# Performance work log

Hardware: AMD Instinct MI355X
Metric: run time of the kernel (lower is better)

The kernel has to match this reference:

```python
import jax, jax.numpy as jnp
import numpy as np

D_MODEL = 768
D_INNER = 1536
D_STATE = 16
D_CONV = 4
DT_RANK = 48
N_LAYER = 4
VOCAB = 32000
B, L = 2, 1024


def rmsnorm(x, w, eps=1e-5):
    return x * jax.lax.rsqrt(jnp.mean(x * x, axis=-1, keepdims=True) + eps) * w


def depthwise_causal_conv(u, w):
    # u: (b, l, d_in), w: (d_in, k). torch pads both sides then truncates to l,
    # which equals left-pad by k-1 (causal).
    b, l, d = u.shape
    k = w.shape[1]
    up = jnp.pad(u, ((0, 0), (k - 1, 0), (0, 0)))
    out = jnp.zeros_like(u)
    for i in range(k):
        out = out + up[:, i:i + l, :] * w[:, i]
    return out


def selective_scan(u, delta, A, Bm, C, Dp):
    # u,delta: (b,l,d_in); A: (d_in,n); Bm,C: (b,l,n); Dp: (d_in,)
    dA = jnp.exp(delta[..., None] * A)                      # (b,l,d,n)
    dBu = delta[..., None] * Bm[:, :, None, :] * u[..., None]

    def step(h, inp):
        dA_t, dBu_t, C_t = inp
        h = dA_t * h + dBu_t                                 # (b,d,n)
        y = jnp.einsum('bdn,bn->bd', h, C_t)
        return h, y

    h0 = jnp.zeros_like(dA[:, 0])
    xs = (jnp.moveaxis(dA, 1, 0), jnp.moveaxis(dBu, 1, 0), jnp.moveaxis(C, 1, 0))
    _, ys = jax.lax.scan(step, h0, xs)                       # (l,b,d)
    return jnp.moveaxis(ys, 0, 1) + u * Dp


def setup_inputs() -> dict:
    key = jax.random.key(0)
    ks = jax.random.split(key, 16)
    s = lambda fan: 1.0 / np.sqrt(fan)
    inp = {}
    inp['text_input'] = jax.random.randint(ks[0], (B, L), 0, VOCAB)
    inp['visual_input'] = jax.random.normal(ks[1], (B, L, D_MODEL), dtype=jnp.float32)
    inp['embedding'] = jax.random.normal(ks[2], (VOCAB, D_MODEL), dtype=jnp.float32) * 0.02
    inp['norm_w'] = jnp.ones((N_LAYER, D_MODEL), dtype=jnp.float32)
    inp['norm_f_w'] = jnp.ones((D_MODEL,), dtype=jnp.float32)
    inp['in_proj_w'] = jax.random.normal(ks[3], (N_LAYER, 2 * D_INNER, D_MODEL)) * s(D_MODEL)
    inp['in_proj2_w'] = jax.random.normal(ks[4], (N_LAYER, D_INNER, D_MODEL)) * s(D_MODEL)
    inp['conv_w'] = jax.random.normal(ks[5], (N_LAYER, D_INNER, D_CONV)) * s(D_CONV)
    inp['conv_b'] = jax.random.normal(ks[6], (N_LAYER, D_INNER)) * 0.01
    inp['x_proj_w'] = jax.random.normal(ks[7], (N_LAYER, DT_RANK + D_STATE, D_INNER)) * s(D_INNER)
    inp['c_proj_w'] = jax.random.normal(ks[8], (N_LAYER, D_STATE, D_INNER)) * s(D_INNER)
    inp['dt_proj_w'] = jax.random.normal(ks[9], (N_LAYER, D_INNER, DT_RANK)) * s(DT_RANK)
    inp['dt_proj_b'] = jax.random.normal(ks[10], (N_LAYER, D_INNER)) * 0.01
    A = jnp.tile(jnp.arange(1, D_STATE + 1, dtype=jnp.float32)[None, :], (D_INNER, 1))
    inp['A_log'] = jnp.tile(jnp.log(A)[None], (N_LAYER, 1, 1))
    inp['D'] = jnp.ones((N_LAYER, D_INNER), dtype=jnp.float32)
    inp['out_proj_w'] = jax.random.normal(ks[11], (N_LAYER, D_MODEL, D_INNER)) * s(D_INNER)
    return inp


def reference(text_input, visual_input, embedding, norm_w, norm_f_w, in_proj_w,
              in_proj2_w, conv_w, conv_b, x_proj_w, c_proj_w, dt_proj_w,
              dt_proj_b, A_log, D, out_proj_w):
    x = embedding[text_input]  # (b,l,d_model)
    n_layer = A_log.shape[0]
    l = x.shape[1]
    for i in range(n_layer):
        q = rmsnorm(x, norm_w[i])
        v = rmsnorm(visual_input, norm_w[i])
        xr = q @ in_proj_w[i].T                               # (b,l,2*d_inner)
        vin = v @ in_proj2_w[i].T                             # (b,l,d_inner)
        t, res = jnp.split(xr, 2, axis=-1)
        t = depthwise_causal_conv(t, conv_w[i]) + conv_b[i]
        t = jax.nn.silu(t)
        # ssm
        A = -jnp.exp(A_log[i])
        x_dbl = t @ x_proj_w[i].T                             # (b,l,dt_rank+n)
        delta, Bm = jnp.split(x_dbl, [DT_RANK], axis=-1)
        C = vin @ c_proj_w[i].T                               # (b,l,n)
        delta = jax.nn.softplus(delta @ dt_proj_w[i].T + dt_proj_b[i])
        y = selective_scan(t, delta, A, Bm, C, D[i])
        y = y * jax.nn.silu(res)
        x = y @ out_proj_w[i].T + x
    x = rmsnorm(x, norm_f_w)
    return x @ embedding.T  # tied lm_head -> (b,l,vocab)
```

## Files before the change

### kernel.cpp

```cpp
#include <hip/hip_runtime.h>
#include <hip/hip_bf16.h>
#include <math.h>

#define B_ 2
#define L_ 1024
#define DM 768
#define DI 1536
#define DS 16
#define DR 48
#define NL 4
#define VOC 32000
#define BL (B_*L_)
#define NCH 32
#define LCH (L_/NCH)
#define NXD 80
#define DTILE 8

typedef __attribute__((ext_vector_type(8))) short short8;
typedef __attribute__((ext_vector_type(4))) float f32x4;

__device__ __forceinline__ float sigmoidf_(float x){ return 1.f/(1.f+expf(-x)); }
__device__ __forceinline__ float siluf_(float x){ return x*sigmoidf_(x); }
__device__ __forceinline__ float softplusf_(float x){ return fmaxf(x,0.f) + log1pf(expf(-fabsf(x))); }
__device__ __forceinline__ unsigned short f2bf(float f){
    unsigned u = __float_as_uint(f);
    u += 0x7FFFu + ((u >> 16) & 1u);
    return (unsigned short)(u >> 16);
}
__device__ __forceinline__ float bf2f(unsigned short h){
    return __uint_as_float((unsigned)h << 16);
}
__device__ __forceinline__ void gload_lds16(const unsigned short* g, unsigned short* l){
    __builtin_amdgcn_global_load_lds(
        (const __attribute__((address_space(1))) void*)g,
        (__attribute__((address_space(3))) void*)l, 16, 0, 0);
}
__device__ __forceinline__ short8 lds_frag(const unsigned short* buf, int row, int kb){
    return *(const short8*)&buf[row*64 + ((kb ^ (row & 7)) << 3)];
}

__global__ void cast_bf16_kernel(const float* __restrict__ in, unsigned short* __restrict__ out, int n4)
{
    for (int i = blockIdx.x*256 + threadIdx.x; i < n4; i += gridDim.x*256) {
        float4 v = ((const float4*)in)[i];
        ushort4 o;
        o.x = f2bf(v.x); o.y = f2bf(v.y); o.z = f2bf(v.z); o.w = f2bf(v.w);
        ((ushort4*)out)[i] = o;
    }
}

__global__ void embed_kernel(const int* __restrict__ idx, const float* __restrict__ emb,
                             float* __restrict__ x)
{
    int i = blockIdx.x*256 + threadIdx.x;
    if (i >= BL*DM) return;
    int c = i % DM; int bl = i / DM;
    x[i] = emb[(size_t)idx[bl]*DM + c];
}

__global__ void rmsnorm_bf_kernel(const float* __restrict__ in, const float* __restrict__ w,
                                  unsigned short* __restrict__ out)
{
    int row = blockIdx.x;
    const float* xr = in + (size_t)row*DM;
    float ss = 0.f;
    for (int c = threadIdx.x; c < DM; c += 256) { float v = xr[c]; ss += v*v; }
    #pragma unroll
    for (int o = 32; o > 0; o >>= 1) ss += __shfl_down(ss, o, 64);
    __shared__ float red[4];
    if ((threadIdx.x & 63) == 0) red[threadIdx.x >> 6] = ss;
    __syncthreads();
    float tot = red[0] + red[1] + red[2] + red[3];
    float scale = rsqrtf(tot * (1.f/DM) + 1e-5f);
    for (int c = threadIdx.x; c < DM; c += 256)
        out[(size_t)row*DM + c] = f2bf(xr[c]*scale*w[c]);
}

__global__ void prep_layer(
    const float* __restrict__ x, const float* __restrict__ vis, const float* __restrict__ w,
    unsigned short* __restrict__ qh, unsigned short* __restrict__ ql,
    unsigned short* __restrict__ vh, unsigned short* __restrict__ vl,
    const float* __restrict__ s1, unsigned short* __restrict__ h1, unsigned short* __restrict__ l1, int n1,
    const float* __restrict__ s2, unsigned short* __restrict__ h2, unsigned short* __restrict__ l2, int n2,
    const float* __restrict__ s3, unsigned short* __restrict__ h3, unsigned short* __restrict__ l3, int n3)
{
    if (blockIdx.x < 2*BL) {
        int row = blockIdx.x;
        bool first = row < BL;
        int r = first ? row : row - BL;
        const float* xr = (first ? x : vis) + (size_t)r*DM;
        unsigned short* oh = (first ? qh : vh) + (size_t)r*DM;
        unsigned short* ol = (first ? ql : vl) + (size_t)r*DM;
        float ss = 0.f;
        for (int c = threadIdx.x; c < DM; c += 256) { float v = xr[c]; ss += v*v; }
        #pragma unroll
        for (int o = 32; o > 0; o >>= 1) ss += __shfl_down(ss, o, 64);
        __shared__ float red[4];
        if ((threadIdx.x & 63) == 0) red[threadIdx.x >> 6] = ss;
        __syncthreads();
        float tot = red[0] + red[1] + red[2] + red[3];
        float scale = rsqrtf(tot * (1.f/DM) + 1e-5f);
        for (int c = threadIdx.x; c < DM; c += 256) {
            float v = xr[c]*scale*w[c];
            unsigned short h = f2bf(v);
            oh[c] = h;
            ol[c] = f2bf(v - bf2f(h));
        }
    } else {
        int total = n1 + n2 + n3;
        int nblk = gridDim.x - 2*BL;
        for (int i = (blockIdx.x - 2*BL)*256 + threadIdx.x; i < total; i += nblk*256) {
            const float* s; unsigned short *h, *l; int j;
            if (i < n1)           { s = s1; h = h1; l = l1; j = i; }
            else if (i < n1 + n2) { s = s2; h = h2; l = l2; j = i - n1; }
            else                  { s = s3; h = h3; l = l3; j = i - n1 - n2; }
            float4 v = ((const float4*)s)[j];
            ushort4 hh, ll;
            hh.x = f2bf(v.x); ll.x = f2bf(v.x - bf2f(hh.x));
            hh.y = f2bf(v.y); ll.y = f2bf(v.y - bf2f(hh.y));
            hh.z = f2bf(v.z); ll.z = f2bf(v.z - bf2f(hh.z));
            hh.w = f2bf(v.w); ll.w = f2bf(v.w - bf2f(hh.w));
            ((ushort4*)h)[j] = hh;
            ((ushort4*)l)[j] = ll;
        }
    }
}

__global__ __launch_bounds__(512) void gemm_head8(
    const unsigned short* __restrict__ A, int lda,
    const unsigned short* __restrict__ W, int ldb,
    float* __restrict__ C, int ldc, int K)
{
    __shared__ unsigned short As[2][256*64];
    __shared__ unsigned short Bs[2][256*64];
    const int tid = threadIdx.x;
    const int bm = blockIdx.y*256, bn = blockIdx.x*256;
    const int l  = tid & 63;
    const int w  = tid >> 6;
    const int wm = w >> 2, wn = w & 3;
    const int lr = l & 15, lg = l >> 4;

    auto stage = [&](int t, int db) {
        int k0 = t*64;
        #pragma unroll
        for (int i = 0; i < 4; i++) {
            int c = i*512 + tid;
            int row = c >> 3, kb = c & 7;
            int kbs = (kb ^ (row & 7)) << 3;
            gload_lds16(A + (size_t)(bm+row)*lda + k0 + kbs, &As[db][c*8]);
        }
        #pragma unroll
        for (int i = 0; i < 4; i++) {
            int c = i*512 + tid;
            int row = c >> 3, kb = c & 7;
            int kbs = (kb ^ (row & 7)) << 3;
            gload_lds16(W + (size_t)(bn+row)*ldb + k0 + kbs, &Bs[db][c*8]);
        }
    };

    f32x4 zero4 = {0.f, 0.f, 0.f, 0.f};
    f32x4 acc[8][4];
    #pragma unroll
    for (int m = 0; m < 8; m++)
        #pragma unroll
        for (int n = 0; n < 4; n++) acc[m][n] = zero4;

    const int NT = K/64;
    stage(0, 0);
    stage(1, 1);

    for (int t = 0; t < NT; t++) {
        int cur = t & 1;
        if (t + 1 < NT) { asm volatile("s_waitcnt vmcnt(8)" ::: "memory"); }
        else            { asm volatile("s_waitcnt vmcnt(0)" ::: "memory"); }
        __builtin_amdgcn_s_barrier();
        __builtin_amdgcn_sched_barrier(0);

        const unsigned short* Ab = As[cur];
        const unsigned short* Bb = Bs[cur];
        short8 bf0[4], bf1[4];
        #pragma unroll
        for (int n = 0; n < 4; n++) {
            int row = wn*64 + n*16 + lr;
            bf0[n] = lds_frag(Bb, row, lg);
            bf1[n] = lds_frag(Bb, row, 4 + lg);
        }
        #pragma unroll
        for (int m = 0; m < 8; m++) {
            int row = wm*128 + m*16 + lr;
            short8 a0 = lds_frag(Ab, row, lg);
            short8 a1 = lds_frag(Ab, row, 4 + lg);
            __builtin_amdgcn_s_setprio(1);
            #pragma unroll
            for (int n = 0; n < 4; n++) {
                acc[m][n] = __builtin_amdgcn_mfma_f32_16x16x32_bf16(a0, bf0[n], acc[m][n], 0, 0, 0);
                acc[m][n] = __builtin_amdgcn_mfma_f32_16x16x32_bf16(a1, bf1[n], acc[m][n], 0, 0, 0);
            }
            __builtin_amdgcn_s_setprio(0);
        }
        __builtin_amdgcn_sched_barrier(0);
        __builtin_amdgcn_s_barrier();
        if (t + 2 < NT) stage(t + 2, cur);
    }

    #pragma unroll
    for (int m = 0; m < 8; m++)
        #pragma unroll
        for (int n = 0; n < 4; n++) {
            int col = bn + wn*64 + n*16 + lr;
            #pragma unroll
            for (int r = 0; r < 4; r++) {
                int rowi = bm + wm*128 + m*16 + lg*4 + r;
                C[(size_t)rowi*ldc + col] = acc[m][n][r];
            }
        }
}

__global__ __launch_bounds__(512) void gemm_mfma2p_dual(
    const unsigned short* __restrict__ Ah1, const unsigned short* __restrict__ Al1,
    const unsigned short* __restrict__ Wh1, const unsigned short* __restrict__ Wl1,
    float* __restrict__ C1, int ldc1, int nb1,
    const unsigned short* __restrict__ Ah2, const unsigned short* __restrict__ Al2,
    const unsigned short* __restrict__ Wh2, const unsigned short* __restrict__ Wl2,
    float* __restrict__ C2, int ldc2,
    int lda, int ldb, int K)
{
    __shared__ unsigned short AsH[2][128*64];
    __shared__ unsigned short AsL[2][128*64];
    __shared__ unsigned short BsH[2][128*64];
    __shared__ unsigned short BsL[2][128*64];
    const int tid = threadIdx.x;
    const int bx = blockIdx.x;
    const bool first = bx < nb1;
    const unsigned short* Ah = first ? Ah1 : Ah2;
    const unsigned short* Al = first ? Al1 : Al2;
    const unsigned short* Wh = first ? Wh1 : Wh2;
    const unsigned short* Wl = first ? Wl1 : Wl2;
    float* C  = first ? C1 : C2;
    const int ldc = first ? ldc1 : ldc2;
    const int bn = (first ? bx : bx - nb1)*128;
    const int bm = blockIdx.y*128;
    const int l  = tid & 63;
    const int w  = tid >> 6;
    const int wm = w >> 2, wn = w & 3;
    const int lr = l & 15, lg = l >> 4;

    auto stage = [&](int t, int db) {
        int k0 = t*64;
        #pragma unroll
        for (int i = 0; i < 2; i++) {
            int c = i*512 + tid;
            int row = c >> 3, kb = c & 7;
            int kbs = (kb ^ (row & 7)) << 3;
            const size_t ao = (size_t)(bm+row)*lda + k0 + kbs;
            const size_t bo = (size_t)(bn+row)*ldb + k0 + kbs;
            gload_lds16(Ah + ao, &AsH[db][c*8]);
            gload_lds16(Al + ao, &AsL[db][c*8]);
            gload_lds16(Wh + bo, &BsH[db][c*8]);
            gload_lds16(Wl + bo, &BsL[db][c*8]);
        }
    };

    f32x4 zero4 = {0.f, 0.f, 0.f, 0.f};
    f32x4 acc[4][2];
    #pragma unroll
    for (int m = 0; m < 4; m++)
        #pragma unroll
        for (int n = 0; n < 2; n++) acc[m][n] = zero4;

    const int NT = K/64;
    stage(0, 0);
    stage(1, 1);

    for (int t = 0; t < NT; t++) {
        int cur = t & 1;
        if (t + 1 < NT) { asm volatile("s_waitcnt vmcnt(8)" ::: "memory"); }
        else            { asm volatile("s_waitcnt vmcnt(0)" ::: "memory"); }
        __builtin_amdgcn_s_barrier();
        __builtin_amdgcn_sched_barrier(0);

        const unsigned short* AbH = AsH[cur];
        const unsigned short* AbL = AsL[cur];
        const unsigned short* BbH = BsH[cur];
        const unsigned short* BbL = BsL[cur];

        #pragma unroll
        for (int kk = 0; kk < 2; kk++) {
            short8 ah[4], al[4], bh[2], bl[2];
            #pragma unroll
            for (int m = 0; m < 4; m++) {
                int row = wm*64 + m*16 + lr;
                ah[m] = lds_frag(AbH, row, kk*4 + lg);
                al[m] = lds_frag(AbL, row, kk*4 + lg);
            }
            #pragma unroll
            for (int n = 0; n < 2; n++) {
                int row = wn*32 + n*16 + lr;
                bh[n] = lds_frag(BbH, row, kk*4 + lg);
                bl[n] = lds_frag(BbL, row, kk*4 + lg);
            }
            __builtin_amdgcn_s_setprio(1);
            #pragma unroll
            for (int m = 0; m < 4; m++)
                #pragma unroll
                for (int n = 0; n < 2; n++) {
                    acc[m][n] = __builtin_amdgcn_mfma_f32_16x16x32_bf16(al[m], bh[n], acc[m][n], 0, 0, 0);
                    acc[m][n] = __builtin_amdgcn_mfma_f32_16x16x32_bf16(ah[m], bl[n], acc[m][n], 0, 0, 0);
                    acc[m][n] = __builtin_amdgcn_mfma_f32_16x16x32_bf16(ah[m], bh[n], acc[m][n], 0, 0, 0);
                }
            __builtin_amdgcn_s_setprio(0);
        }
        __builtin_amdgcn_sched_barrier(0);
        __builtin_amdgcn_s_barrier();
        if (t + 2 < NT) stage(t + 2, cur);
    }

    #pragma unroll
    for (int m = 0; m < 4; m++)
        #pragma unroll
        for (int n = 0; n < 2; n++) {
            int col = bn + wn*32 + n*16 + lr;
            #pragma unroll
            for (int r = 0; r < 4; r++) {
                int rowi = bm + wm*64 + m*16 + lg*4 + r;
                C[(size_t)rowi*ldc + col] = acc[m][n][r];
            }
        }
}

template<int EPI>
__device__ __forceinline__ void mfma2_body(
    const unsigned short* __restrict__ Ah, const unsigned short* __restrict__ Alo, int lda,
    const unsigned short* __restrict__ Wh, const unsigned short* __restrict__ Wlo, int ldb,
    float* __restrict__ C, int ldc, const float* __restrict__ extra,
    int K, int bm, int bn,
    unsigned short* Ash, unsigned short* Asl, unsigned short* Bsh, unsigned short* Bsl)
{
    const int tid = threadIdx.x;
    const int l  = tid & 63;
    const int w  = tid >> 6;
    const int wr = (w >> 1)*64, wc = (w & 1)*64;
    const int lr = l & 15, lg = l >> 4;

    f32x4 zero4 = {0.f, 0.f, 0.f, 0.f};
    f32x4 acc[4][4];
    #pragma unroll
    for (int m = 0; m < 4; m++)
        #pragma unroll
        for (int n = 0; n < 4; n++) acc[m][n] = zero4;

    for (int k0 = 0; k0 < K; k0 += 64) {
        __syncthreads();
        #pragma unroll
        for (int i = 0; i < 4; i++) {
            int c   = i*256 + tid;
            int row = c >> 3;
            int kb  = c & 7;
            int kbs = (kb ^ (row & 7)) << 3;
            const size_t ao = (size_t)(bm+row)*lda + k0 + kbs;
            const size_t bo = (size_t)(bn+row)*ldb + k0 + kbs;
            gload_lds16(Ah  + ao, &Ash[c*8]);
            gload_lds16(Alo + ao, &Asl[c*8]);
            gload_lds16(Wh  + bo, &Bsh[c*8]);
            gload_lds16(Wlo + bo, &Bsl[c*8]);
        }
        __syncthreads();
        #pragma unroll
        for (int kk = 0; kk < 2; kk++) {
            short8 ah[4], al[4], bh[4], bl[4];
            #pragma unroll
            for (int m = 0; m < 4; m++) {
                int row = wr + m*16 + lr;
                ah[m] = lds_frag(Ash, row, kk*4 + lg);
                al[m] = lds_frag(Asl, row, kk*4 + lg);
            }
            #pragma unroll
            for (int n = 0; n < 4; n++) {
                int row = wc + n*16 + lr;
                bh[n] = lds_frag(Bsh, row, kk*4 + lg);
                bl[n] = lds_frag(Bsl, row, kk*4 + lg);
            }
            #pragma unroll
            for (int m = 0; m < 4; m++)
                #pragma unroll
                for (int n = 0; n < 4; n++) {
                    acc[m][n] = __builtin_amdgcn_mfma_f32_16x16x32_bf16(al[m], bh[n], acc[m][n], 0, 0, 0);
                    acc[m][n] = __builtin_amdgcn_mfma_f32_16x16x32_bf16(ah[m], bl[n], acc[m][n], 0, 0, 0);
                    acc[m][n] = __builtin_amdgcn_mfma_f32_16x16x32_bf16(ah[m], bh[n], acc[m][n], 0, 0, 0);
                }
        }
    }

    #pragma unroll
    for (int m = 0; m < 4; m++)
        #pragma unroll
        for (int n = 0; n < 4; n++) {
            int col = bn + wc + n*16 + lr;
            #pragma unroll
            for (int r = 0; r < 4; r++) {
                int rowi = bm + wr + m*16 + lg*4 + r;
                float v = acc[m][n][r];
                if (EPI == 1) v += extra[(size_t)rowi*ldc + col];
                C[(size_t)rowi*ldc + col] = v;
            }
        }
}

template<int EPI>
__global__ __launch_bounds__(256) void gemm_mfma2(
    const unsigned short* __restrict__ Ah, const unsigned short* __restrict__ Alo, int lda,
    const unsigned short* __restrict__ Wh, const unsigned short* __restrict__ Wlo, int ldb,
    float* __restrict__ C, int ldc, const float* __restrict__ extra, int K)
{
    __shared__ unsigned short Ash[128*64];
    __shared__ unsigned short Asl[128*64];
    __shared__ unsigned short Bsh[128*64];
    __shared__ unsigned short Bsl[128*64];
    mfma2_body<EPI>(Ah, Alo, lda, Wh, Wlo, ldb, C, ldc, extra, K,
                    blockIdx.y*128, blockIdx.x*128, Ash, Asl, Bsh, Bsl);
}

template<int EPI>
__global__ __launch_bounds__(256) void gemm_tile(
    const float* __restrict__ A, int lda,
    const float* __restrict__ W, int ldb,
    float* __restrict__ C, int ldc,
    const float* __restrict__ extra,
    int K)
{
    __shared__ float As[8][128];
    __shared__ float Bs[8][128];
    const int bm = blockIdx.y * 128;
    const int bn = blockIdx.x * 128;
    const int tid = threadIdx.x;
    const int lr = tid >> 1;
    const int lh = (tid & 1) * 4;
    const int tr = tid >> 4;
    const int tc = tid & 15;

    float acc[8][8];
    #pragma unroll
    for (int i = 0; i < 8; i++)
        #pragma unroll
        for (int j = 0; j < 8; j++) acc[i][j] = 0.f;

    const float* Arow = A + (size_t)(bm + lr)*lda + lh;
    const float* Wrow = W + (size_t)(bn + lr)*ldb + lh;

    for (int k0 = 0; k0 < K; k0 += 8) {
        float4 av = *(const float4*)(Arow + k0);
        float4 wv = *(const float4*)(Wrow + k0);
        __syncthreads();
        As[lh+0][lr] = av.x; As[lh+1][lr] = av.y; As[lh+2][lr] = av.z; As[lh+3][lr] = av.w;
        Bs[lh+0][lr] = wv.x; Bs[lh+1][lr] = wv.y; Bs[lh+2][lr] = wv.z; Bs[lh+3][lr] = wv.w;
        __syncthreads();
        #pragma unroll
        for (int k = 0; k < 8; k++) {
            float a[8], b[8];
            *(float4*)(a)   = *(const float4*)&As[k][tr*8];
            *(float4*)(a+4) = *(const float4*)&As[k][tr*8+4];
            *(float4*)(b)   = *(const float4*)&Bs[k][tc*8];
            *(float4*)(b+4) = *(const float4*)&Bs[k][tc*8+4];
            #pragma unroll
            for (int i = 0; i < 8; i++)
                #pragma unroll
                for (int j = 0; j < 8; j++)
                    acc[i][j] = fmaf(a[i], b[j], acc[i][j]);
        }
    }

    #pragma unroll
    for (int i = 0; i < 8; i++) {
        int row = bm + tr*8 + i;
        float* crow = C + (size_t)row*ldc + bn + tc*8;
        float v[8];
        if (EPI == 2) {
            const float* bia = extra + bn + tc*8;
            #pragma unroll
            for (int j = 0; j < 8; j++) v[j] = softplusf_(acc[i][j] + bia[j]);
        } else {
            #pragma unroll
            for (int j = 0; j < 8; j++) v[j] = acc[i][j];
        }
        *(float4*)(crow)   = make_float4(v[0],v[1],v[2],v[3]);
        *(float4*)(crow+4) = make_float4(v[4],v[5],v[6],v[7]);
    }
}

__global__ __launch_bounds__(256) void gemm_skinny2(
    const float* __restrict__ A1, const float* __restrict__ A2, int lda,
    const float* __restrict__ W1, const float* __restrict__ W2, int ldb,
    float* __restrict__ outx, int K)
{
    __shared__ float As[64][36];
    __shared__ float Ws[16][36];
    int tid = threadIdx.x;
    int bx = blockIdx.x;
    bool isC = (bx == 4);
    const float* A = isC ? A2 : A1;
    const float* W = isC ? W2 : W1;
    int bn = isC ? 0 : bx*16;
    int colbase = isC ? 64 : bx*16;
    int bm = blockIdx.y*64;
    int ar = tid >> 2, ak = (tid & 3)*8;
    int wr = tid >> 4, wk = (tid & 15)*2;
    int tr = tid >> 4, tc = tid & 15;

    float acc[4] = {0.f,0.f,0.f,0.f};
    for (int k0 = 0; k0 < K; k0 += 32) {
        float4 a0 = *(const float4*)(A + (size_t)(bm+ar)*lda + k0 + ak);
        float4 a1 = *(const float4*)(A + (size_t)(bm+ar)*lda + k0 + ak + 4);
        float2 wv = *(const float2*)(W + (size_t)(bn+wr)*ldb + k0 + wk);
        __syncthreads();
        *(float4*)&As[ar][ak]   = a0;
        *(float4*)&As[ar][ak+4] = a1;
        Ws[wr][wk] = wv.x; Ws[wr][wk+1] = wv.y;
        __syncthreads();
        #pragma unroll
        for (int k = 0; k < 32; k += 4) {
            float4 wv4 = *(const float4*)&Ws[tc][k];
            #pragma unroll
            for (int i = 0; i < 4; i++) {
                float4 av4 = *(const float4*)&As[tr*4+i][k];
                acc[i] = fmaf(av4.x, wv4.x, acc[i]);
                acc[i] = fmaf(av4.y, wv4.y, acc[i]);
                acc[i] = fmaf(av4.z, wv4.z, acc[i]);
                acc[i] = fmaf(av4.w, wv4.w, acc[i]);
            }
        }
    }
    #pragma unroll
    for (int i = 0; i < 4; i++)
        outx[(size_t)(bm + tr*4 + i)*NXD + colbase + tc] = acc[i];
}

__global__ void conv_silu_kernel(const float* __restrict__ xr, const float* __restrict__ cw,
                                 const float* __restrict__ cb, float* __restrict__ t)
{
    int i = blockIdx.x*256 + threadIdx.x;
    if (i >= BL*DI) return;
    int d = i % DI; int bl = i / DI; int l = bl % L_; int b = bl / L_;
    const float* base = xr + (size_t)b*L_*(2*DI);
    float acc = cb[d];
    #pragma unroll
    for (int q = 0; q < 4; q++) {
        int ll = l - 3 + q;
        if (ll >= 0) acc = fmaf(base[(size_t)ll*(2*DI) + d], cw[d*4+q], acc);
    }
    t[i] = siluf_(acc);
}

__global__ __launch_bounds__(256) void scan_fused(
    const float* __restrict__ delta, const float* __restrict__ t,
    const float* __restrict__ xdbl,
    const float* __restrict__ A_log, const float* __restrict__ Dp,
    const float* __restrict__ xr,
    unsigned short* __restrict__ zh, unsigned short* __restrict__ zl)
{
    __shared__ float P_lds[256*17];
    __shared__ float S_lds[256*17];
    int blk = blockIdx.x;
    int b  = blk / (DI/DTILE);
    int d0 = (blk % (DI/DTILE))*DTILE;
    int tid = threadIdx.x;
    int dl = tid & (DTILE-1), c = tid / DTILE;
    int d = d0 + dl;

    float Ad[16];
    #pragma unroll
    for (int n = 0; n < 16; n++) Ad[n] = -expf(A_log[d*16+n]);

    float P[16], S[16];
    #pragma unroll
    for (int n = 0; n < 16; n++) { P[n] = 1.f; S[n] = 0.f; }
    for (int s = 0; s < LCH; s++) {
        int bl = b*L_ + c*LCH + s;
        float dt = delta[(size_t)bl*DI + d];
        float u  = t[(size_t)bl*DI + d];
        const float4* Bp4 = (const float4*)(xdbl + (size_t)bl*NXD + 48);
        float Bv[16];
        #pragma unroll
        for (int q = 0; q < 4; q++) {
            float4 bv = Bp4[q];
            Bv[q*4+0]=bv.x; Bv[q*4+1]=bv.y; Bv[q*4+2]=bv.z; Bv[q*4+3]=bv.w;
        }
        float du = dt*u;
        #pragma unroll
        for (int n = 0; n < 16; n++) {
            float a = expf(dt*Ad[n]);
            P[n] *= a;
            S[n] = fmaf(a, S[n], du*Bv[n]);
        }
    }
    #pragma unroll
    for (int n = 0; n < 16; n++) { P_lds[tid*17+n] = P[n]; S_lds[tid*17+n] = S[n]; }
    __syncthreads();

    if (tid < DTILE*16) {
        int dl2 = tid >> 4, n2 = tid & 15;
        float h = 0.f;
        for (int cc = 0; cc < NCH; cc++) {
            int slot = cc*DTILE + dl2;
            float p = P_lds[slot*17 + n2];
            float s = S_lds[slot*17 + n2];
            S_lds[slot*17 + n2] = h;
            h = fmaf(p, h, s);
        }
    }
    __syncthreads();

    float h[16];
    #pragma unroll
    for (int n = 0; n < 16; n++) h[n] = S_lds[tid*17+n];
    float Dd = Dp[d];
    for (int s = 0; s < LCH; s++) {
        int bl = b*L_ + c*LCH + s;
        float dt = delta[(size_t)bl*DI + d];
        float u  = t[(size_t)bl*DI + d];
        const float4* Bp4 = (const float4*)(xdbl + (size_t)bl*NXD + 48);
        const float4* Cp4 = (const float4*)(xdbl + (size_t)bl*NXD + 64);
        float Bv[16], Cv[16];
        #pragma unroll
        for (int q = 0; q < 4; q++) {
            float4 bv = Bp4[q]; float4 cv = Cp4[q];
            Bv[q*4+0]=bv.x; Bv[q*4+1]=bv.y; Bv[q*4+2]=bv.z; Bv[q*4+3]=bv.w;
            Cv[q*4+0]=cv.x; Cv[q*4+1]=cv.y; Cv[q*4+2]=cv.z; Cv[q*4+3]=cv.w;
        }
        float du = dt*u;
        float y = 0.f;
        #pragma unroll
        for (int n = 0; n < 16; n++) {
            float a = expf(dt*Ad[n]);
            h[n] = fmaf(a, h[n], du*Bv[n]);
            y = fmaf(h[n], Cv[n], y);
        }
        y = fmaf(u, Dd, y);
        float r = xr[(size_t)bl*(2*DI) + DI + d];
        float zv = y * siluf_(r);
        unsigned short hh = f2bf(zv);
        zh[(size_t)bl*DI + d] = hh;
        zl[(size_t)bl*DI + d] = f2bf(zv - bf2f(hh));
    }
}

extern "C" void kernel_launch(void* const* d_in, const int* in_sizes, int n_in,
                              void* d_out, int out_size, void* d_ws, size_t ws_size,
                              hipStream_t stream)
{
    const int*   text     = (const int*)  d_in[0];
    const float* visual   = (const float*)d_in[1];
    const float* emb      = (const float*)d_in[2];
    const float* norm_w   = (const float*)d_in[3];
    const float* norm_f_w = (const float*)d_in[4];
    const float* in_proj  = (const float*)d_in[5];
    const float* in_proj2 = (const float*)d_in[6];
    const float* conv_w   = (const float*)d_in[7];
    const float* conv_b   = (const float*)d_in[8];
    const float* x_proj   = (const float*)d_in[9];
    const float* c_proj   = (const float*)d_in[10];
    const float* dt_w     = (const float*)d_in[11];
    const float* dt_b     = (const float*)d_in[12];
    const float* A_log    = (const float*)d_in[13];
    const float* Dp       = (const float*)d_in[14];
    const float* out_proj = (const float*)d_in[15];
    float* out = (float*)d_out;

    float* ws = (float*)d_ws;
    size_t off = 0;
    float* x     = ws + off; off += (size_t)BL*DM;
    float* xr    = ws + off; off += (size_t)BL*2*DI;
    float* vin   = ws + off; off += (size_t)BL*DI;
    float* tb    = ws + off; off += (size_t)BL*DI;
    float* dl    = ws + off; off += (size_t)BL*DI;
    float* xdbl  = ws + off; off += (size_t)BL*NXD;

    unsigned short* bfb = (unsigned short*)(ws + off);
    size_t bo = 0;
    unsigned short* emb_bf = bfb + bo; bo += (size_t)VOC*DM;
    unsigned short* wA_h   = bfb + bo; bo += (size_t)2*DI*DM;
    unsigned short* wA_l   = bfb + bo; bo += (size_t)2*DI*DM;
    unsigned short* wB_h   = bfb + bo; bo += (size_t)DI*DM;
    unsigned short* wB_l   = bfb + bo; bo += (size_t)DI*DM;
    unsigned short* wO_h   = bfb + bo; bo += (size_t)DM*DI;
    unsigned short* wO_l   = bfb + bo; bo += (size_t)DM*DI;
    unsigned short* q_h    = bfb + bo; bo += (size_t)BL*DM;
    unsigned short* q_l    = bfb + bo; bo += (size_t)BL*DM;
    unsigned short* v_h    = bfb + bo; bo += (size_t)BL*DM;
    unsigned short* v_l    = bfb + bo; bo += (size_t)BL*DM;
    unsigned short* z_h    = bfb + bo; bo += (size_t)BL*DI;
    unsigned short* z_l    = bfb + bo; bo += (size_t)BL*DI;
    unsigned short* xn_bf  = bfb + bo; bo += (size_t)BL*DM;

    dim3 blk(256);

    cast_bf16_kernel<<<dim3(2048), blk, 0, stream>>>(emb, emb_bf, VOC*DM/4);

    embed_kernel<<<dim3((BL*DM)/256), blk, 0, stream>>>(text, emb, x);

    for (int i = 0; i < NL; i++) {
        const float* nw = norm_w + (size_t)i*DM;

        prep_layer<<<dim3(2*BL + 1024), blk, 0, stream>>>(
            x, visual, nw, q_h, q_l, v_h, v_l,
            in_proj  + (size_t)i*2*DI*DM, wA_h, wA_l, 2*DI*DM/4,
            in_proj2 + (size_t)i*DI*DM,   wB_h, wB_l, DI*DM/4,
            out_proj + (size_t)i*DM*DI,   wO_h, wO_l, DM*DI/4);

        gemm_mfma2p_dual<<<dim3(2*DI/128 + DI/128, BL/128), dim3(512), 0, stream>>>(
            q_h, q_l, wA_h, wA_l, xr, 2*DI, 2*DI/128,
            v_h, v_l, wB_h, wB_l, vin, DI,
            DM, DM, DM);

        conv_silu_kernel<<<dim3((BL*DI)/256), blk, 0, stream>>>(
            xr, conv_w + (size_t)i*DI*4, conv_b + (size_t)i*DI, tb);

        gemm_skinny2<<<dim3(5, BL/64), blk, 0, stream>>>(
            tb, vin, DI, x_proj + (size_t)i*(DR+DS)*DI, c_proj + (size_t)i*DS*DI, DI,
            xdbl, DI);

        gemm_tile<2><<<dim3(DI/128, BL/128), blk, 0, stream>>>(
            xdbl, NXD, dt_w + (size_t)i*DI*DR, DR, dl, DI, dt_b + (size_t)i*DI, DR);

        scan_fused<<<dim3(B_*DI/DTILE), blk, 0, stream>>>(
            dl, tb, xdbl, A_log + (size_t)i*DI*DS, Dp + (size_t)i*DI, xr, z_h, z_l);

        gemm_mfma2<1><<<dim3(DM/128, BL/128), blk, 0, stream>>>(
            z_h, z_l, DI, wO_h, wO_l, DI, x, DM, x, DI);
    }

    rmsnorm_bf_kernel<<<dim3(BL), blk, 0, stream>>>(x, norm_f_w, xn_bf);
    gemm_head8<<<dim3(VOC/256, BL/256), dim3(512), 0, stream>>>(
        xn_bf, DM, emb_bf, DM, out, VOC, DM);
}
```

Measured before the change: 1.589 ms.

## Fuse causal conv+SiLU into skinny GEMM and scan, drop separate conv kernel

Removes the standalone depthwise causal conv + SiLU kernel and its intermediate buffer. The x_proj skinny GEMM now loads xr tiles with a 3-row halo into LDS and computes conv+SiLU on the fly. The scan kernel recomputes the conv output from xr in both passes. This saves one launch and a write plus reread of the BL*DI intermediate. In exchange the scan does four strided xr reads and a sigmoid per step, twice, and the GEMM gets an extra sync and more work per tile.

```diff
diff --git a/kernel.cpp b/kernel.cpp
--- a/kernel.cpp
+++ b/kernel.cpp
@@ -488,16 +488,20 @@
 }
 
 __global__ __launch_bounds__(256) void gemm_skinny2(
-    const float* __restrict__ A1, const float* __restrict__ A2, int lda,
+    const float* __restrict__ xr,
+    const float* __restrict__ vin,
+    const float* __restrict__ cw, const float* __restrict__ cb,
     const float* __restrict__ W1, const float* __restrict__ W2, int ldb,
     float* __restrict__ outx, int K)
 {
-    __shared__ float As[64][36];
+    __shared__ float Ar[68][36];
+    __shared__ float Ac[64][36];
     __shared__ float Ws[16][36];
+    __shared__ float cwS[32][4];
+    __shared__ float cbS[32];
     int tid = threadIdx.x;
     int bx = blockIdx.x;
     bool isC = (bx == 4);
-    const float* A = isC ? A2 : A1;
     const float* W = isC ? W2 : W1;
     int bn = isC ? 0 : bx*16;
     int colbase = isC ? 64 : bx*16;
@@ -505,23 +509,66 @@
     int ar = tid >> 2, ak = (tid & 3)*8;
     int wr = tid >> 4, wk = (tid & 15)*2;
     int tr = tid >> 4, tc = tid & 15;
+    bool halo_ok = (bm % L_) != 0;
 
     float acc[4] = {0.f,0.f,0.f,0.f};
     for (int k0 = 0; k0 < K; k0 += 32) {
-        float4 a0 = *(const float4*)(A + (size_t)(bm+ar)*lda + k0 + ak);
-        float4 a1 = *(const float4*)(A + (size_t)(bm+ar)*lda + k0 + ak + 4);
+        float4 a0, a1, h0, h1, cwv;
+        float cbv = 0.f;
+        if (isC) {
+            a0 = *(const float4*)(vin + (size_t)(bm+ar)*DI + k0 + ak);
+            a1 = *(const float4*)(vin + (size_t)(bm+ar)*DI + k0 + ak + 4);
+        } else {
+            a0 = *(const float4*)(xr + (size_t)(bm+ar)*(2*DI) + k0 + ak);
+            a1 = *(const float4*)(xr + (size_t)(bm+ar)*(2*DI) + k0 + ak + 4);
+            if (tid < 12) {
+                if (halo_ok) {
+                    h0 = *(const float4*)(xr + (size_t)(bm-3+(tid>>2))*(2*DI) + k0 + (tid&3)*8);
+                    h1 = *(const float4*)(xr + (size_t)(bm-3+(tid>>2))*(2*DI) + k0 + (tid&3)*8 + 4);
+                } else {
+                    h0 = make_float4(0.f,0.f,0.f,0.f);
+                    h1 = make_float4(0.f,0.f,0.f,0.f);
+                }
+            }
+            if (tid < 32) {
+                cwv = *(const float4*)(cw + (size_t)(k0+tid)*4);
+                cbv = cb[k0+tid];
+            }
+        }
         float2 wv = *(const float2*)(W + (size_t)(bn+wr)*ldb + k0 + wk);
         __syncthreads();
-        *(float4*)&As[ar][ak]   = a0;
-        *(float4*)&As[ar][ak+4] = a1;
+        if (isC) {
+            *(float4*)&Ar[ar][ak]   = a0;
+            *(float4*)&Ar[ar][ak+4] = a1;
+        } else {
+            *(float4*)&Ar[3+ar][ak]   = a0;
+            *(float4*)&Ar[3+ar][ak+4] = a1;
+            if (tid < 12) {
+                *(float4*)&Ar[tid>>2][(tid&3)*8]     = h0;
+                *(float4*)&Ar[tid>>2][(tid&3)*8 + 4] = h1;
+            }
+            if (tid < 32) { *(float4*)&cwS[tid][0] = cwv; cbS[tid] = cbv; }
+        }
         Ws[wr][wk] = wv.x; Ws[wr][wk+1] = wv.y;
         __syncthreads();
+        if (!isC) {
+            #pragma unroll
+            for (int e = tid; e < 64*32; e += 256) {
+                int r = e >> 5, k = e & 31;
+                float a = cbS[k];
+                #pragma unroll
+                for (int q = 0; q < 4; q++) a = fmaf(Ar[r+q][k], cwS[k][q], a);
+                Ac[r][k] = siluf_(a);
+            }
+            __syncthreads();
+        }
+        const float (*Au)[36] = isC ? (const float (*)[36])Ar : (const float (*)[36])Ac;
         #pragma unroll
         for (int k = 0; k < 32; k += 4) {
             float4 wv4 = *(const float4*)&Ws[tc][k];
             #pragma unroll
             for (int i = 0; i < 4; i++) {
-                float4 av4 = *(const float4*)&As[tr*4+i][k];
+                float4 av4 = *(const float4*)&Au[tr*4+i][k];
                 acc[i] = fmaf(av4.x, wv4.x, acc[i]);
                 acc[i] = fmaf(av4.y, wv4.y, acc[i]);
                 acc[i] = fmaf(av4.z, wv4.z, acc[i]);
@@ -534,26 +581,11 @@
         outx[(size_t)(bm + tr*4 + i)*NXD + colbase + tc] = acc[i];
 }
 
-__global__ void conv_silu_kernel(const float* __restrict__ xr, const float* __restrict__ cw,
-                                 const float* __restrict__ cb, float* __restrict__ t)
-{
-    int i = blockIdx.x*256 + threadIdx.x;
-    if (i >= BL*DI) return;
-    int d = i % DI; int bl = i / DI; int l = bl % L_; int b = bl / L_;
-    const float* base = xr + (size_t)b*L_*(2*DI);
-    float acc = cb[d];
-    #pragma unroll
-    for (int q = 0; q < 4; q++) {
-        int ll = l - 3 + q;
-        if (ll >= 0) acc = fmaf(base[(size_t)ll*(2*DI) + d], cw[d*4+q], acc);
-    }
-    t[i] = siluf_(acc);
-}
-
 __global__ __launch_bounds__(256) void scan_fused(
-    const float* __restrict__ delta, const float* __restrict__ t,
+    const float* __restrict__ delta,
     const float* __restrict__ xdbl,
     const float* __restrict__ A_log, const float* __restrict__ Dp,
+    const float* __restrict__ cw, const float* __restrict__ cb,
     const float* __restrict__ xr,
     unsigned short* __restrict__ zh, unsigned short* __restrict__ zl)
 {
@@ -569,14 +601,25 @@
     float Ad[16];
     #pragma unroll
     for (int n = 0; n < 16; n++) Ad[n] = -expf(A_log[d*16+n]);
+    float cw4[4];
+    #pragma unroll
+    for (int q = 0; q < 4; q++) cw4[q] = cw[d*4+q];
+    float cbv = cb[d];
 
     float P[16], S[16];
     #pragma unroll
     for (int n = 0; n < 16; n++) { P[n] = 1.f; S[n] = 0.f; }
     for (int s = 0; s < LCH; s++) {
-        int bl = b*L_ + c*LCH + s;
+        int lloc = c*LCH + s;
+        int bl = b*L_ + lloc;
         float dt = delta[(size_t)bl*DI + d];
-        float u  = t[(size_t)bl*DI + d];
+        float tv = cbv;
+        #pragma unroll
+        for (int q = 0; q < 4; q++) {
+            int ll = lloc - 3 + q;
+            if (ll >= 0) tv = fmaf(xr[(size_t)(b*L_ + ll)*(2*DI) + d], cw4[q], tv);
+        }
+        float u = siluf_(tv);
         const float4* Bp4 = (const float4*)(xdbl + (size_t)bl*NXD + 48);
         float Bv[16];
         #pragma unroll
@@ -614,9 +657,16 @@
     for (int n = 0; n < 16; n++) h[n] = S_lds[tid*17+n];
     float Dd = Dp[d];
     for (int s = 0; s < LCH; s++) {
-        int bl = b*L_ + c*LCH + s;
+        int lloc = c*LCH + s;
+        int bl = b*L_ + lloc;
         float dt = delta[(size_t)bl*DI + d];
-        float u  = t[(size_t)bl*DI + d];
+        float tv = cbv;
+        #pragma unroll
+        for (int q = 0; q < 4; q++) {
+            int ll = lloc - 3 + q;
+            if (ll >= 0) tv = fmaf(xr[(size_t)(b*L_ + ll)*(2*DI) + d], cw4[q], tv);
+        }
+        float u = siluf_(tv);
         const float4* Bp4 = (const float4*)(xdbl + (size_t)bl*NXD + 48);
         const float4* Cp4 = (const float4*)(xdbl + (size_t)bl*NXD + 64);
         float Bv[16], Cv[16];
@@ -670,7 +720,6 @@
     float* x     = ws + off; off += (size_t)BL*DM;
     float* xr    = ws + off; off += (size_t)BL*2*DI;
     float* vin   = ws + off; off += (size_t)BL*DI;
-    float* tb    = ws + off; off += (size_t)BL*DI;
     float* dl    = ws + off; off += (size_t)BL*DI;
     float* xdbl  = ws + off; off += (size_t)BL*NXD;
 
@@ -699,6 +748,8 @@
 
     for (int i = 0; i < NL; i++) {
         const float* nw = norm_w + (size_t)i*DM;
+        const float* cwL = conv_w + (size_t)i*DI*4;
+        const float* cbL = conv_b + (size_t)i*DI;
 
         prep_layer<<<dim3(2*BL + 1024), blk, 0, stream>>>(
             x, visual, nw, q_h, q_l, v_h, v_l,
@@ -711,18 +762,17 @@
             v_h, v_l, wB_h, wB_l, vin, DI,
             DM, DM, DM);
 
-        conv_silu_kernel<<<dim3((BL*DI)/256), blk, 0, stream>>>(
-            xr, conv_w + (size_t)i*DI*4, conv_b + (size_t)i*DI, tb);
-
         gemm_skinny2<<<dim3(5, BL/64), blk, 0, stream>>>(
-            tb, vin, DI, x_proj + (size_t)i*(DR+DS)*DI, c_proj + (size_t)i*DS*DI, DI,
+            xr, vin, cwL, cbL,
+            x_proj + (size_t)i*(DR+DS)*DI, c_proj + (size_t)i*DS*DI, DI,
             xdbl, DI);
 
         gemm_tile<2><<<dim3(DI/128, BL/128), blk, 0, stream>>>(
             xdbl, NXD, dt_w + (size_t)i*DI*DR, DR, dl, DI, dt_b + (size_t)i*DI, DR);
 
         scan_fused<<<dim3(B_*DI/DTILE), blk, 0, stream>>>(
-            dl, tb, xdbl, A_log + (size_t)i*DI*DS, Dp + (size_t)i*DI, xr, z_h, z_l);
+            dl, xdbl, A_log + (size_t)i*DI*DS, Dp + (size_t)i*DI,
+            cwL, cbL, xr, z_h, z_l);
 
         gemm_mfma2<1><<<dim3(DM/128, BL/128), blk, 0, stream>>>(
             z_h, z_l, DI, wO_h, wO_l, DI, x, DM, x, DI);
```

New measurement: 1.926 ms. +21.2%, slower.
